# Kernel optimization log

Measured on AMD Instinct MI355X. Metric: run time of the kernel, lower is better.

The kernel has to match this reference:

```python
import jax, jax.numpy as jnp
import numpy as np

EMBED_DIM = 768
NUM_HEADS = 12
HEAD_DIM = EMBED_DIM // NUM_HEADS


def setup_inputs() -> dict:
    key = jax.random.key(0)
    k_x, k_wqkv, k_bqkv, k_wo, k_bo = jax.random.split(key, 5)
    B, S, D = 4, 2048, EMBED_DIM
    bound = 1.0 / np.sqrt(D)
    x = jax.random.normal(k_x, (B, S, D), dtype=jnp.float32)
    # nn.Linear weights: torch stores [out, in]; we keep same layout and use x @ W.T
    W_qkv = jax.random.uniform(k_wqkv, (3 * D, D), jnp.float32, -bound, bound)
    b_qkv = jax.random.uniform(k_bqkv, (3 * D,), jnp.float32, -bound, bound)
    W_out = jax.random.uniform(k_wo, (D, D), jnp.float32, -bound, bound)
    b_out = jax.random.uniform(k_bo, (D,), jnp.float32, -bound, bound)
    return {"x": x, "W_qkv": W_qkv, "b_qkv": b_qkv, "W_out": W_out, "b_out": b_out}


def reference(x, W_qkv, b_qkv, W_out, b_out):
    B, S, D = x.shape
    H, Hd = NUM_HEADS, HEAD_DIM
    qkv = x @ W_qkv.T + b_qkv                       # [B,S,3D]
    qkv = qkv.reshape(B, S, H, 3 * Hd).transpose(0, 2, 1, 3)  # [B,H,S,3Hd]
    q, k, v = jnp.split(qkv, 3, axis=-1)            # each [B,H,S,Hd]
    scale = Hd ** -0.5
    scores = jnp.einsum("bhsd,bhtd->bhst", q, k) * scale  # [B,H,S,S]
    weights = jax.nn.softmax(scores, axis=-1)
    ctx = jnp.einsum("bhst,bhtd->bhsd", weights, v)       # [B,H,S,Hd]
    ctx = ctx.transpose(0, 2, 1, 3).reshape(B, S, D)      # [B,S,D]
    return ctx @ W_out.T + b_out
```

## Files before the change

kernel.cpp:

```cpp
#include <hip/hip_runtime.h>
#include <hip/hip_bf16.h>
#include <stdint.h>
#include <math.h>

typedef unsigned short u16;
typedef __attribute__((ext_vector_type(8))) short short8;
typedef __attribute__((ext_vector_type(4))) short short4v;
typedef __attribute__((ext_vector_type(4))) float f32x4;
typedef __attribute__((ext_vector_type(16))) float f32x16;
typedef __attribute__((ext_vector_type(4))) unsigned int u32x4;
typedef __attribute__((ext_vector_type(2))) unsigned int u32x2;

#define NB 4
#define NS 2048
#define NH 12
#define HD 64
#define ND 768
#define ND3 2304

#define QSCALE 0.18033688f

__device__ __forceinline__ u16 f2bf(float f) {
    unsigned int u = __float_as_uint(f);
    unsigned int r = u + 0x7fffu + ((u >> 16) & 1u);
    return (u16)(r >> 16);
}

#define XN4   1572864
#define WQN4  442368
#define WON4  147456
__global__ __launch_bounds__(256) void castall(const float* __restrict__ x,
                                               const float* __restrict__ wq,
                                               const float* __restrict__ wo,
                                               u16* __restrict__ xb,
                                               u16* __restrict__ wqb,
                                               u16* __restrict__ wob) {
    int i = blockIdx.x * 256 + threadIdx.x;
    const float* s; u16* d; int j;
    if (i < XN4) { s = x; d = xb; j = i; }
    else if (i < XN4 + WQN4) { s = wq; d = wqb; j = i - XN4; }
    else if (i < XN4 + WQN4 + WON4) { s = wo; d = wob; j = i - XN4 - WQN4; }
    else return;
    float4 v = ((const float4*)s)[j];
    ushort4 o;
    o.x = f2bf(v.x); o.y = f2bf(v.y); o.z = f2bf(v.z); o.w = f2bf(v.w);
    ((ushort4*)d)[j] = o;
}

__global__ __launch_bounds__(256, 3) void gemm_qkv(const u16* __restrict__ A,
                                                   const u16* __restrict__ Bw,
                                                   const float* __restrict__ bias,
                                                   u16* __restrict__ Qg,
                                                   u16* __restrict__ Kg,
                                                   u16* __restrict__ Vtg) {
    __shared__ u16 lds[10240];
    const int tid = threadIdx.x;
    const int w = tid >> 6, l = tid & 63;
    const int lam = l & 15, quad = l >> 4;
    const int wm = w >> 1, wn = w & 1;
    const int bm = blockIdx.x * 128;
    const int hh = blockIdx.y;
    const int bn = hh * 192;
    const int K = ND;

    f32x4 acc[4][6];
#pragma unroll
    for (int i = 0; i < 4; i++)
#pragma unroll
        for (int j = 0; j < 6; j++) { f32x4 z = {0.f, 0.f, 0.f, 0.f}; acc[i][j] = z; }

    const u16* gp[5];
    u16* sp[5];
#pragma unroll
    for (int i = 0; i < 5; i++) {
        int c = w * 5 + i;
        if (c < 8) { gp[i] = A + (size_t)(bm + c * 16 + lam) * K + quad * 8; sp[i] = lds + c * 512; }
        else { int nf = c - 8; gp[i] = Bw + (size_t)(bn + nf * 16 + lam) * K + quad * 8; sp[i] = lds + 4096 + nf * 512; }
    }

    u32x4 rg[5];
#pragma unroll
    for (int i = 0; i < 5; i++) rg[i] = *(const u32x4*)gp[i];

    for (int k0 = 0; k0 < K; k0 += 32) {
        __syncthreads();
#pragma unroll
        for (int i = 0; i < 5; i++) *(u32x4*)(sp[i] + (size_t)l * 8) = rg[i];
        __syncthreads();
        if (k0 + 32 < K) {
#pragma unroll
            for (int i = 0; i < 5; i++) rg[i] = *(const u32x4*)(gp[i] + k0 + 32);
        }
        short8 a[4];
#pragma unroll
        for (int i = 0; i < 4; i++) a[i] = *(const short8*)(lds + (wm * 4 + i) * 512 + l * 8);
#pragma unroll
        for (int half = 0; half < 2; half++) {
            short8 b[3];
#pragma unroll
            for (int j = 0; j < 3; j++) b[j] = *(const short8*)(lds + 4096 + (wn * 6 + half * 3 + j) * 512 + l * 8);
#pragma unroll
            for (int mf = 0; mf < 4; mf++)
#pragma unroll
                for (int j = 0; j < 3; j++)
                    acc[mf][half * 3 + j] = __builtin_amdgcn_mfma_f32_16x16x32_bf16(a[mf], b[j], acc[mf][half * 3 + j], 0, 0, 0);
        }
    }

#pragma unroll
    for (int nf = 0; nf < 6; nf++) {
        int nloc = wn * 96 + nf * 16;
        int rgn = nloc / 64;
        int d = (nloc % 64) + lam;
        float bv = bias[bn + nloc + lam];
        if (rgn == 2) {
#pragma unroll
            for (int mf = 0; mf < 4; mf++) {
                int m0 = bm + wm * 64 + mf * 16 + quad * 4;
                int bq = m0 >> 11, s0 = m0 & 2047;
                ushort4 o;
                o.x = f2bf(acc[mf][nf][0] + bv);
                o.y = f2bf(acc[mf][nf][1] + bv);
                o.z = f2bf(acc[mf][nf][2] + bv);
                o.w = f2bf(acc[mf][nf][3] + bv);
                *(ushort4*)(Vtg + ((size_t)((bq * NH + hh) * HD + d)) * NS + s0) = o;
            }
        } else {
            u16* dst = (rgn == 0) ? Qg : Kg;
            const float sc = (rgn == 0) ? QSCALE : 1.0f;
#pragma unroll
            for (int mf = 0; mf < 4; mf++)
#pragma unroll
                for (int r = 0; r < 4; r++) {
                    int m = bm + wm * 64 + mf * 16 + quad * 4 + r;
                    int bq = m >> 11, s = m & 2047;
                    dst[((size_t)((bq * NH + hh) * NS + s)) * HD + d] = f2bf((acc[mf][nf][r] + bv) * sc);
                }
        }
    }
}

__global__ __launch_bounds__(256, 3) void attn(const u16* __restrict__ Qg,
                                               const u16* __restrict__ Kg,
                                               const u16* __restrict__ Vtg,
                                               u16* __restrict__ ctx) {
    __shared__ u16 kt_lds[8192];
    __shared__ u16 vt_lds[8192];
    __shared__ float linv[128];
    const int tid = threadIdx.x;
    const int w = tid >> 6, L = tid & 63;
    const int r5 = L & 31, h = L >> 5;
    const int bid = blockIdx.x;
    const int qt = bid / 48, bh = bid % 48;
    const int b = bh / NH, hd = bh % NH;
    const u16* Qh = Qg + (size_t)bh * NS * HD;
    const u16* Kh = Kg + (size_t)bh * NS * HD;
    const u16* Vh = Vtg + (size_t)bh * HD * NS;

    const int qbase = qt * 128 + w * 32;

    short8 qf[4];
#pragma unroll
    for (int s = 0; s < 4; s++)
        qf[s] = *(const short8*)(Qh + (size_t)(qbase + r5) * HD + s * 16 + h * 8);

    f32x16 ot[2];
#pragma unroll
    for (int hg = 0; hg < 2; hg++)
#pragma unroll
        for (int r = 0; r < 16; r++) ot[hg][r] = 0.f;
    float lacc = 0.f;

    const u16* gp[8];
    u16* sp[8];
    int step;
    if (w < 2) {
#pragma unroll
        for (int i = 0; i < 8; i++) {
            int c = w * 8 + i, kg = c >> 2, s = c & 3;
            gp[i] = Kh + (size_t)(kg * 32 + r5) * HD + s * 16 + h * 8;
            sp[i] = kt_lds + c * 512;
        }
        step = 128 * HD;
    } else {
#pragma unroll
        for (int i = 0; i < 8; i++) {
            int c = (w - 2) * 8 + i;
            gp[i] = Vh + (size_t)((c >> 3) * 32 + r5) * NS + (c & 7) * 16 + h * 8;
            sp[i] = vt_lds + c * 512;
        }
        step = 128;
    }

    u32x4 rg[8];
#pragma unroll
    for (int i = 0; i < 8; i++) { rg[i] = *(const u32x4*)gp[i]; gp[i] += step; }

    for (int kt = 0; kt < 16; kt++) {
        __syncthreads();
#pragma unroll
        for (int i = 0; i < 8; i++) *(u32x4*)(sp[i] + (size_t)L * 8) = rg[i];
        __syncthreads();

        if (kt < 15) {
#pragma unroll
            for (int i = 0; i < 8; i++) { rg[i] = *(const u32x4*)gp[i]; gp[i] += step; }
        }

#pragma unroll
        for (int kg = 0; kg < 4; kg++) {
            f32x16 st;
#pragma unroll
            for (int r = 0; r < 16; r++) st[r] = 0.f;
#pragma unroll
            for (int s = 0; s < 4; s++) {
                short8 kf = *(const short8*)(kt_lds + (kg * 4 + s) * 512 + L * 8);
                st = __builtin_amdgcn_mfma_f32_32x32x16_bf16(kf, qf[s], st, 0, 0, 0);
            }

            unsigned int q8[8];
#pragma unroll
            for (int i = 0; i < 8; i++) {
                float e0 = __builtin_amdgcn_exp2f(st[2 * i + 0]);
                float e1 = __builtin_amdgcn_exp2f(st[2 * i + 1]);
                lacc += e0 + e1;
                unsigned int u0 = __float_as_uint(e0) + 0x8000u;
                unsigned int u1 = __float_as_uint(e1) + 0x8000u;
                q8[i] = __builtin_amdgcn_perm(u1, u0, 0x07060302u);
            }
            u32x2 s02 = __builtin_amdgcn_permlane32_swap(q8[0], q8[2], false, false);
            u32x2 s13 = __builtin_amdgcn_permlane32_swap(q8[1], q8[3], false, false);
            u32x2 s46 = __builtin_amdgcn_permlane32_swap(q8[4], q8[6], false, false);
            u32x2 s57 = __builtin_amdgcn_permlane32_swap(q8[5], q8[7], false, false);
            union { u32x4 u; short8 s; } af0, af1;
            af0.u = (u32x4){s02.x, s13.x, s02.y, s13.y};
            af1.u = (u32x4){s46.x, s57.x, s46.y, s57.y};

#pragma unroll
            for (int hg = 0; hg < 2; hg++) {
                short8 vf0 = *(const short8*)(vt_lds + (hg * 8 + kg * 2 + 0) * 512 + L * 8);
                short8 vf1 = *(const short8*)(vt_lds + (hg * 8 + kg * 2 + 1) * 512 + L * 8);
                ot[hg] = __builtin_amdgcn_mfma_f32_32x32x16_bf16(af0.s, vf0, ot[hg], 0, 0, 0);
                ot[hg] = __builtin_amdgcn_mfma_f32_32x32x16_bf16(af1.s, vf1, ot[hg], 0, 0, 0);
            }
        }
    }

    float lg = lacc + __shfl_xor(lacc, 32);
    linv[w * 32 + r5] = 1.0f / lg;
    __builtin_amdgcn_s_waitcnt(0xc07f);

    float sc[16];
#pragma unroll
    for (int r = 0; r < 16; r++) sc[r] = linv[w * 32 + (r & 3) + 8 * (r >> 2) + 4 * h];
#pragma unroll
    for (int hg = 0; hg < 2; hg++) {
#pragma unroll
        for (int r = 0; r < 16; r++) {
            int q = qbase + (r & 3) + 8 * (r >> 2) + 4 * h;
            ctx[(size_t)(b * NS + q) * ND + hd * HD + hg * 32 + r5] = f2bf(ot[hg][r] * sc[r]);
        }
    }
}

__global__ __launch_bounds__(256) void gemm_out(const u16* __restrict__ A,
                                                const u16* __restrict__ Bw,
                                                const float* __restrict__ bias,
                                                float* __restrict__ out) {
    __shared__ u16 lds[7168];
    const int tid = threadIdx.x;
    const int w = tid >> 6, l = tid & 63;
    const int lam = l & 15, quad = l >> 4;
    const int wm = w >> 1, wn = w & 1;
    const int bm = blockIdx.x * 128, bn = blockIdx.y * 96;
    const int K = ND;

    f32x4 acc[4][3];
#pragma unroll
    for (int i = 0; i < 4; i++)
#pragma unroll
        for (int j = 0; j < 3; j++) { f32x4 z = {0.f, 0.f, 0.f, 0.f}; acc[i][j] = z; }

    const u16* gp[4];
    u16* sp[4];
#pragma unroll
    for (int i = 0; i < 4; i++) {
        int c = w * 4 + i;
        if (c >= 14) c -= 14;
        if (c < 8) { gp[i] = A + (size_t)(bm + c * 16 + lam) * K + quad * 8; sp[i] = lds + c * 512; }
        else { int nf = c - 8; gp[i] = Bw + (size_t)(bn + nf * 16 + lam) * K + quad * 8; sp[i] = lds + 4096 + nf * 512; }
    }

    u32x4 rg[4];
#pragma unroll
    for (int i = 0; i < 4; i++) rg[i] = *(const u32x4*)gp[i];

    for (int k0 = 0; k0 < K; k0 += 32) {
        __syncthreads();
#pragma unroll
        for (int i = 0; i < 4; i++) *(u32x4*)(sp[i] + (size_t)l * 8) = rg[i];
        __syncthreads();
        if (k0 + 32 < K) {
#pragma unroll
            for (int i = 0; i < 4; i++) rg[i] = *(const u32x4*)(gp[i] + k0 + 32);
        }
        short8 a[4], b[3];
#pragma unroll
        for (int i = 0; i < 4; i++) a[i] = *(const short8*)(lds + (wm * 4 + i) * 512 + l * 8);
#pragma unroll
        for (int j = 0; j < 3; j++) b[j] = *(const short8*)(lds + 4096 + (wn * 3 + j) * 512 + l * 8);
#pragma unroll
        for (int mf = 0; mf < 4; mf++)
#pragma unroll
            for (int j = 0; j < 3; j++)
                acc[mf][j] = __builtin_amdgcn_mfma_f32_16x16x32_bf16(a[mf], b[j], acc[mf][j], 0, 0, 0);
    }

#pragma unroll
    for (int nf = 0; nf < 3; nf++) {
        int n = bn + wn * 48 + nf * 16 + lam;
        float bv = bias[n];
#pragma unroll
        for (int mf = 0; mf < 4; mf++)
#pragma unroll
            for (int r = 0; r < 4; r++) {
                int m = bm + wm * 64 + mf * 16 + quad * 4 + r;
                out[(size_t)m * ND + n] = acc[mf][nf][r] + bv;
            }
    }
}

extern "C" void kernel_launch(void* const* d_in, const int* in_sizes, int n_in,
                              void* d_out, int out_size, void* d_ws, size_t ws_size,
                              hipStream_t stream) {
    const float* x    = (const float*)d_in[0];
    const float* Wqkv = (const float*)d_in[1];
    const float* bqkv = (const float*)d_in[2];
    const float* Wout = (const float*)d_in[3];
    const float* bout = (const float*)d_in[4];
    float* out = (float*)d_out;

    u16* p = (u16*)d_ws;
    u16* xb    = p; p += 6291456;
    u16* wqkvb = p; p += 1769472;
    u16* wob   = p; p += 589824;
    u16* Qg    = p; p += 6291456;
    u16* Kg    = p; p += 6291456;
    u16* Vtg   = p; p += 6291456;
    u16* ctx   = p; p += 6291456;

    castall<<<8448, 256, 0, stream>>>(x, Wqkv, Wout, xb, wqkvb, wob);
    gemm_qkv<<<dim3(64, 12), 256, 0, stream>>>(xb, wqkvb, bqkv, Qg, Kg, Vtg);
    attn<<<768, 256, 0, stream>>>(Qg, Kg, Vtg, ctx);
    gemm_out<<<dim3(64, 8), 256, 0, stream>>>(ctx, wob, bout, out);
}
```

Before: 229.8 us.

## Double-buffer GEMM LDS tiles with direct global-to-LDS async loads

Both projection GEMMs now load tiles straight from global memory into LDS with global_load_lds instead of staging through registers. LDS is double-buffered, so the next k-slice is fetched while MFMAs run on the current one, and each iteration needs one barrier instead of two. This frees the staging registers and overlaps memory with compute, at the cost of twice the LDS per block (possibly lower occupancy) and depending on the lane-to-LDS address mapping of the 16-byte direct loads matching the old layout.

```diff
diff --git a/kernel.cpp b/kernel.cpp
--- a/kernel.cpp
+++ b/kernel.cpp
@@ -24,6 +24,12 @@
     unsigned int u = __float_as_uint(f);
     unsigned int r = u + 0x7fffu + ((u >> 16) & 1u);
     return (u16)(r >> 16);
+}
+
+__device__ __forceinline__ void gload16(const u16* g, u16* s) {
+    __builtin_amdgcn_global_load_lds(
+        (const __attribute__((address_space(1))) unsigned int*)(const void*)g,
+        (__attribute__((address_space(3))) unsigned int*)(void*)s, 16, 0, 0);
 }
 
 #define XN4   1572864
@@ -53,7 +59,7 @@
                                                    u16* __restrict__ Qg,
                                                    u16* __restrict__ Kg,
                                                    u16* __restrict__ Vtg) {
-    __shared__ u16 lds[10240];
+    __shared__ u16 lds[2][10240];
     const int tid = threadIdx.x;
     const int w = tid >> 6, l = tid & 63;
     const int lam = l & 15, quad = l >> 4;
@@ -70,41 +76,42 @@
         for (int j = 0; j < 6; j++) { f32x4 z = {0.f, 0.f, 0.f, 0.f}; acc[i][j] = z; }
 
     const u16* gp[5];
-    u16* sp[5];
+    int so[5];
 #pragma unroll
     for (int i = 0; i < 5; i++) {
         int c = w * 5 + i;
-        if (c < 8) { gp[i] = A + (size_t)(bm + c * 16 + lam) * K + quad * 8; sp[i] = lds + c * 512; }
-        else { int nf = c - 8; gp[i] = Bw + (size_t)(bn + nf * 16 + lam) * K + quad * 8; sp[i] = lds + 4096 + nf * 512; }
-    }
-
-    u32x4 rg[5];
-#pragma unroll
-    for (int i = 0; i < 5; i++) rg[i] = *(const u32x4*)gp[i];
-
+        if (c < 8) { gp[i] = A + (size_t)(bm + c * 16 + lam) * K + quad * 8; so[i] = c * 512; }
+        else { int nf = c - 8; gp[i] = Bw + (size_t)(bn + nf * 16 + lam) * K + quad * 8; so[i] = 4096 + nf * 512; }
+    }
+
+#pragma unroll
+    for (int i = 0; i < 5; i++) gload16(gp[i], &lds[0][so[i]]);
+    asm volatile("s_waitcnt vmcnt(0)" ::: "memory");
+    __syncthreads();
+
+    int cur = 0;
     for (int k0 = 0; k0 < K; k0 += 32) {
-        __syncthreads();
-#pragma unroll
-        for (int i = 0; i < 5; i++) *(u32x4*)(sp[i] + (size_t)l * 8) = rg[i];
-        __syncthreads();
         if (k0 + 32 < K) {
 #pragma unroll
-            for (int i = 0; i < 5; i++) rg[i] = *(const u32x4*)(gp[i] + k0 + 32);
+            for (int i = 0; i < 5; i++) gload16(gp[i] + k0 + 32, &lds[cur ^ 1][so[i]]);
         }
         short8 a[4];
 #pragma unroll
-        for (int i = 0; i < 4; i++) a[i] = *(const short8*)(lds + (wm * 4 + i) * 512 + l * 8);
+        for (int i = 0; i < 4; i++) a[i] = *(const short8*)(&lds[cur][(wm * 4 + i) * 512 + l * 8]);
 #pragma unroll
         for (int half = 0; half < 2; half++) {
             short8 b[3];
 #pragma unroll
-            for (int j = 0; j < 3; j++) b[j] = *(const short8*)(lds + 4096 + (wn * 6 + half * 3 + j) * 512 + l * 8);
+            for (int j = 0; j < 3; j++) b[j] = *(const short8*)(&lds[cur][4096 + (wn * 6 + half * 3 + j) * 512 + l * 8]);
 #pragma unroll
             for (int mf = 0; mf < 4; mf++)
 #pragma unroll
                 for (int j = 0; j < 3; j++)
                     acc[mf][half * 3 + j] = __builtin_amdgcn_mfma_f32_16x16x32_bf16(a[mf], b[j], acc[mf][half * 3 + j], 0, 0, 0);
         }
+        asm volatile("s_waitcnt vmcnt(0)" ::: "memory");
+        __syncthreads();
+        cur ^= 1;
     }
 
 #pragma unroll
@@ -267,7 +274,7 @@
                                                 const u16* __restrict__ Bw,
                                                 const float* __restrict__ bias,
                                                 float* __restrict__ out) {
-    __shared__ u16 lds[7168];
+    __shared__ u16 lds[2][7168];
     const int tid = threadIdx.x;
     const int w = tid >> 6, l = tid & 63;
     const int lam = l & 15, quad = l >> 4;
@@ -282,38 +289,39 @@
         for (int j = 0; j < 3; j++) { f32x4 z = {0.f, 0.f, 0.f, 0.f}; acc[i][j] = z; }
 
     const u16* gp[4];
-    u16* sp[4];
+    int so[4];
 #pragma unroll
     for (int i = 0; i < 4; i++) {
         int c = w * 4 + i;
         if (c >= 14) c -= 14;
-        if (c < 8) { gp[i] = A + (size_t)(bm + c * 16 + lam) * K + quad * 8; sp[i] = lds + c * 512; }
-        else { int nf = c - 8; gp[i] = Bw + (size_t)(bn + nf * 16 + lam) * K + quad * 8; sp[i] = lds + 4096 + nf * 512; }
-    }
-
-    u32x4 rg[4];
-#pragma unroll
-    for (int i = 0; i < 4; i++) rg[i] = *(const u32x4*)gp[i];
-
+        if (c < 8) { gp[i] = A + (size_t)(bm + c * 16 + lam) * K + quad * 8; so[i] = c * 512; }
+        else { int nf = c - 8; gp[i] = Bw + (size_t)(bn + nf * 16 + lam) * K + quad * 8; so[i] = 4096 + nf * 512; }
+    }
+
+#pragma unroll
+    for (int i = 0; i < 4; i++) gload16(gp[i], &lds[0][so[i]]);
+    asm volatile("s_waitcnt vmcnt(0)" ::: "memory");
+    __syncthreads();
+
+    int cur = 0;
     for (int k0 = 0; k0 < K; k0 += 32) {
-        __syncthreads();
-#pragma unroll
-        for (int i = 0; i < 4; i++) *(u32x4*)(sp[i] + (size_t)l * 8) = rg[i];
-        __syncthreads();
         if (k0 + 32 < K) {
 #pragma unroll
-            for (int i = 0; i < 4; i++) rg[i] = *(const u32x4*)(gp[i] + k0 + 32);
+            for (int i = 0; i < 4; i++) gload16(gp[i] + k0 + 32, &lds[cur ^ 1][so[i]]);
         }
         short8 a[4], b[3];
 #pragma unroll
-        for (int i = 0; i < 4; i++) a[i] = *(const short8*)(lds + (wm * 4 + i) * 512 + l * 8);
-#pragma unroll
-        for (int j = 0; j < 3; j++) b[j] = *(const short8*)(lds + 4096 + (wn * 3 + j) * 512 + l * 8);
+        for (int i = 0; i < 4; i++) a[i] = *(const short8*)(&lds[cur][(wm * 4 + i) * 512 + l * 8]);
+#pragma unroll
+        for (int j = 0; j < 3; j++) b[j] = *(const short8*)(&lds[cur][4096 + (wn * 3 + j) * 512 + l * 8]);
 #pragma unroll
         for (int mf = 0; mf < 4; mf++)
 #pragma unroll
             for (int j = 0; j < 3; j++)
                 acc[mf][j] = __builtin_amdgcn_mfma_f32_16x16x32_bf16(a[mf], b[j], acc[mf][j], 0, 0, 0);
+        asm volatile("s_waitcnt vmcnt(0)" ::: "memory");
+        __syncthreads();
+        cur ^= 1;
     }
 
 #pragma unroll
```

Result: no change. 227.8 us (-0.9%).
